# Optimization experiments

Hardware: AMD Instinct MI355X
Metric: run time of the kernel (lower is better)

Reference implementation:

```python
import jax, jax.numpy as jnp
import numpy as np

N1, N2, K = 262144, 65536, 16   # dense points, coarse points, knn neighbors
CIN, COUT = 64, 64              # in_planes, out_planes
EPS = 1e-5


def bn(x, g, b, m, v):
    # eval-mode BatchNorm1d with learned affine and running stats
    return (x - m) * jax.lax.rsqrt(v + EPS) * g + b


def setup_inputs() -> dict:
    key = jax.random.key(0)
    ks = jax.random.split(key, 32)
    u = lambda k, *s: jax.random.normal(k, s, jnp.float32)
    lin = lambda k, o, i: jax.random.normal(k, (o, i), jnp.float32) / np.float32(np.sqrt(i))
    inp = dict(
        p1=u(ks[0], N1, 3), p2=u(ks[1], N2, 3),
        x1=u(ks[2], N1, COUT), x2=u(ks[3], N2, CIN),
        knn_idx=jax.random.randint(ks[4], (N2, K), 0, N1),
        # linear1: Linear(COUT,COUT) + BN + ReLU
        w1=lin(ks[5], COUT, COUT), b1=0.01 * u(ks[6], COUT),
        g1=jnp.ones(COUT), be1=jnp.zeros(COUT),
        m1=0.1 * u(ks[7], COUT), v1=jax.random.uniform(ks[8], (COUT,), minval=0.5, maxval=1.5),
        # linear2: Linear(CIN,COUT) + BN + ReLU
        w2=lin(ks[9], COUT, CIN), b2=0.01 * u(ks[10], COUT),
        g2=jnp.ones(COUT), be2=jnp.zeros(COUT),
        m2=0.1 * u(ks[11], COUT), v2=jax.random.uniform(ks[12], (COUT,), minval=0.5, maxval=1.5),
        # channel_shrinker: Linear(CIN+3,CIN) + BN + ReLU + Linear(CIN,1)
        ws1=lin(ks[13], CIN, CIN + 3), bs1=0.01 * u(ks[14], CIN),
        gs=jnp.ones(CIN), bes=jnp.zeros(CIN),
        ms=0.1 * u(ks[15], CIN), vs=jax.random.uniform(ks[16], (CIN,), minval=0.5, maxval=1.5),
        ws2=lin(ks[17], 1, CIN), bs2=0.01 * u(ks[18], 1),
    )
    return inp


def reference(p1, p2, x1, x2, knn_idx,
              w1, b1, g1, be1, m1, v1,
              w2, b2, g2, be2, m2, v2,
              ws1, bs1, gs, bes, ms, vs, ws2, bs2):
    idx = knn_idx.reshape(-1)                                   # [M] = [N2*K], indices into p1
    # relative position of each knn neighbor to its coarse query point
    p_r = p1[idx].reshape(N2, K, 3) - p2[:, None, :]            # [N2,K,3]
    x2k = jnp.concatenate(
        [p_r, jnp.broadcast_to(x2[:, None, :], (N2, K, CIN))], axis=-1
    ).reshape(N2 * K, CIN + 3)                                  # [M, CIN+3]
    # channel_shrinker MLP -> scalar logit per (coarse, neighbor) pair
    h = jax.nn.relu(bn(x2k @ ws1.T + bs1, gs, bes, ms, vs))     # [M, CIN]
    logit = (h @ ws2.T + bs2)[:, 0]                             # [M]
    # scatter_softmax over variable in-degree groups keyed by dense point idx
    gmax = jax.lax.stop_gradient(jax.ops.segment_max(logit, idx, num_segments=N1))
    e = jnp.exp(logit - gmax[idx])
    denom = jax.ops.segment_sum(e, idx, num_segments=N1)
    prob = e / denom[idx]                                       # [M]
    # linear2(x2), broadcast over K neighbors, weight, scatter-sum to dense points
    up_feat = jax.nn.relu(bn(x2 @ w2.T + b2, g2, be2, m2, v2))  # [N2, COUT]
    weighted = (up_feat[:, None, :] * prob.reshape(N2, K, 1)).reshape(N2 * K, COUT)
    up = jax.ops.segment_sum(weighted, idx, num_segments=N1)    # [N1, COUT]
    # skip branch: linear1(x1)
    y1 = jax.nn.relu(bn(x1 @ w1.T + b1, g1, be1, m1, v1))       # [N1, COUT]
    return y1 + up
```

## Files before the change

### kernel.cpp

```cpp
#include <hip/hip_runtime.h>

#define CN1 262144
#define CN2 65536
#define CK  16
#define CM  (CN2*CK)

typedef unsigned short u16;
typedef unsigned int   u32;
typedef float f32x4 __attribute__((ext_vector_type(4)));

__device__ __forceinline__ float b2f(u16 h) {
    union { u32 u; float f; } v; v.u = ((u32)h) << 16; return v.f;
}
__device__ __forceinline__ u16 f2b(float f) {
    union { float f; u32 u; } v; v.f = f;
    u32 lsb = (v.u >> 16) & 1u;
    return (u16)((v.u + 0x7FFFu + lsb) >> 16);
}

#define W_POS   0
#define W_FT    256
#define W_AS    12544
#define W_BS    12608
#define W_WS2   12672
#define W_A2    12736
#define W_B2    12800
#define W_A1    12864
#define W_B1    12928
#define W_BS2   12992
#define W_MODE  13000
#define W_W1T   13056
#define W_W2T   17152
#define W_JP    21248

__device__ __forceinline__ float ldv(const void* p, size_t i, int bf) {
    return bf ? b2f(((const u16*)p)[i]) : ((const float*)p)[i];
}

#define DECL_ACC8 \
    f32x4 A0={0,0,0,0},A1={0,0,0,0},A2={0,0,0,0},A3={0,0,0,0}, \
          A4={0,0,0,0},A5={0,0,0,0},A6={0,0,0,0},A7={0,0,0,0};

#define FMA4(A, Wv) \
    (A).x = fmaf(xv_, (Wv).x, (A).x); (A).y = fmaf(xv_, (Wv).y, (A).y); \
    (A).z = fmaf(xv_, (Wv).z, (A).z); (A).w = fmaf(xv_, (Wv).w, (A).w);

#define WSTEP8(wtco, ivar, xval) { \
    float xv_ = (xval); \
    const f32x4* wr_ = (const f32x4*)((wtco) + ((size_t)(ivar) << 6)); \
    FMA4(A0, wr_[0])  FMA4(A1, wr_[1])  FMA4(A2, wr_[2])  FMA4(A3, wr_[3]) \
    FMA4(A4, wr_[4])  FMA4(A5, wr_[5])  FMA4(A6, wr_[6])  FMA4(A7, wr_[7]) }

#define GEMV32T(bf, xrow_f, xrow_u4, wtco) \
    if (bf) { \
        const uint4* xu_ = (xrow_u4); \
        _Pragma("unroll 2") \
        for (int ii_ = 0; ii_ < 8; ++ii_) { \
            uint4 xc_ = xu_[ii_]; \
            WSTEP8(wtco, ii_*8+0, b2f((u16)(xc_.x & 0xffffu))) \
            WSTEP8(wtco, ii_*8+1, b2f((u16)(xc_.x >> 16))) \
            WSTEP8(wtco, ii_*8+2, b2f((u16)(xc_.y & 0xffffu))) \
            WSTEP8(wtco, ii_*8+3, b2f((u16)(xc_.y >> 16))) \
            WSTEP8(wtco, ii_*8+4, b2f((u16)(xc_.z & 0xffffu))) \
            WSTEP8(wtco, ii_*8+5, b2f((u16)(xc_.z >> 16))) \
            WSTEP8(wtco, ii_*8+6, b2f((u16)(xc_.w & 0xffffu))) \
            WSTEP8(wtco, ii_*8+7, b2f((u16)(xc_.w >> 16))) \
        } \
    } else { \
        const float4* xf_ = (xrow_f); \
        _Pragma("unroll 2") \
        for (int ii_ = 0; ii_ < 8; ++ii_) { \
            float4 xa_ = xf_[2*ii_], xb_ = xf_[2*ii_+1]; \
            WSTEP8(wtco, ii_*8+0, xa_.x) WSTEP8(wtco, ii_*8+1, xa_.y) \
            WSTEP8(wtco, ii_*8+2, xa_.z) WSTEP8(wtco, ii_*8+3, xa_.w) \
            WSTEP8(wtco, ii_*8+4, xb_.x) WSTEP8(wtco, ii_*8+5, xb_.y) \
            WSTEP8(wtco, ii_*8+6, xb_.z) WSTEP8(wtco, ii_*8+7, xb_.w) \
        } \
    }

#define BNR1(A, av, bv) \
    (A).x = fmaxf(fmaf((A).x,(av).x,(bv).x),0.f); \
    (A).y = fmaxf(fmaf((A).y,(av).y,(bv).y),0.f); \
    (A).z = fmaxf(fmaf((A).z,(av).z,(bv).z),0.f); \
    (A).w = fmaxf(fmaf((A).w,(av).w,(bv).w),0.f);
#define BNR8(aBase, bBase) { \
    const f32x4* av_ = (const f32x4*)(aBase); \
    const f32x4* bv_ = (const f32x4*)(bBase); \
    BNR1(A0,av_[0],bv_[0]) BNR1(A1,av_[1],bv_[1]) \
    BNR1(A2,av_[2],bv_[2]) BNR1(A3,av_[3],bv_[3]) \
    BNR1(A4,av_[4],bv_[4]) BNR1(A5,av_[5],bv_[5]) \
    BNR1(A6,av_[6],bv_[6]) BNR1(A7,av_[7],bv_[7]) }

#define UFQ(q, AL, AH) { uint4 u_ = ufr_[q]; \
    (AL).x = fmaf(pe_, b2f((u16)(u_.x & 0xffffu)), (AL).x); \
    (AL).y = fmaf(pe_, b2f((u16)(u_.x >> 16)),     (AL).y); \
    (AL).z = fmaf(pe_, b2f((u16)(u_.y & 0xffffu)), (AL).z); \
    (AL).w = fmaf(pe_, b2f((u16)(u_.y >> 16)),     (AL).w); \
    (AH).x = fmaf(pe_, b2f((u16)(u_.z & 0xffffu)), (AH).x); \
    (AH).y = fmaf(pe_, b2f((u16)(u_.z >> 16)),     (AH).y); \
    (AH).z = fmaf(pe_, b2f((u16)(u_.w & 0xffffu)), (AH).z); \
    (AH).w = fmaf(pe_, b2f((u16)(u_.w >> 16)),     (AH).w); }

#define STQ(q, AL, AH, dst) { uint4 o_; \
    o_.x = (u32)f2b((AL).x) | ((u32)f2b((AL).y) << 16); \
    o_.y = (u32)f2b((AL).z) | ((u32)f2b((AL).w) << 16); \
    o_.z = (u32)f2b((AH).x) | ((u32)f2b((AH).y) << 16); \
    o_.w = (u32)f2b((AH).z) | ((u32)f2b((AH).w) << 16); \
    ((uint4*)(dst))[q] = o_; }
#define STORE_BF8(dst) \
    STQ(0,A0,A1,dst) STQ(1,A2,A3,dst) STQ(2,A4,A5,dst) STQ(3,A6,A7,dst)
#define STORE_F328(dst) { f32x4* ov_ = (f32x4*)(dst); \
    ov_[0]=A0; ov_[1]=A1; ov_[2]=A2; ov_[3]=A3; \
    ov_[4]=A4; ov_[5]=A5; ov_[6]=A6; ov_[7]=A7; }

__global__ __launch_bounds__(256) void k_prep(
    const void* __restrict__ w1,  const void* __restrict__ b1,  const void* __restrict__ g1,
    const void* __restrict__ be1, const void* __restrict__ m1,  const void* __restrict__ v1,
    const void* __restrict__ w2,  const void* __restrict__ b2,  const void* __restrict__ g2,
    const void* __restrict__ be2, const void* __restrict__ m2,  const void* __restrict__ v2,
    const void* __restrict__ ws1, const void* __restrict__ bs1, const void* __restrict__ gs,
    const void* __restrict__ bes, const void* __restrict__ ms,  const void* __restrict__ vs,
    const void* __restrict__ ws2, const void* __restrict__ bs2, float* __restrict__ wb,
    u32* __restrict__ offsets, u32* __restrict__ cursor)
{
    int b = blockIdx.x;
    int tid = threadIdx.x;
    if (b > 0) {
        offsets[(b - 1) * 256 + tid] = 0u;
        if (b == 1 && tid == 0) *cursor = 0u;
        return;
    }

    u32 w0 = ((const u32*)g1)[0];
    int bf = (w0 != 0x3F800000u) ? 1 : 0;

    for (int t = tid; t < 64*64; t += 256) {
        int i = t >> 6, c = t & 63;
        wb[W_FT  + t] = ldv(ws1, (size_t)c*67 + 3 + i, bf);
        wb[W_W1T + t] = ldv(w1,  (size_t)c*64 + i, bf);
        wb[W_W2T + t] = ldv(w2,  (size_t)c*64 + i, bf);
    }
    for (int t = tid; t < 64*3; t += 256) {
        int j = t / 3, k = t % 3;
        wb[W_POS + t] = ldv(ws1, (size_t)j*67 + k, bf);
    }
    if (tid < 64) {
        float as = ldv(gs, tid, bf) * rsqrtf(ldv(vs, tid, bf) + 1e-5f);
        float bs = (ldv(bs1, tid, bf) - ldv(ms, tid, bf)) * as + ldv(bes, tid, bf);
        float wc = ldv(ws2, tid, bf);
        wb[W_AS + tid] = as;
        wb[W_BS + tid] = bs;
        wb[W_WS2 + tid] = wc;
        float a2 = ldv(g2, tid, bf) * rsqrtf(ldv(v2, tid, bf) + 1e-5f);
        wb[W_A2 + tid] = a2;
        wb[W_B2 + tid] = (ldv(b2, tid, bf) - ldv(m2, tid, bf)) * a2 + ldv(be2, tid, bf);
        float a1 = ldv(g1, tid, bf) * rsqrtf(ldv(v1, tid, bf) + 1e-5f);
        wb[W_A1 + tid] = a1;
        wb[W_B1 + tid] = (ldv(b1, tid, bf) - ldv(m1, tid, bf)) * a1 + ldv(be1, tid, bf);
        wb[W_JP + tid*8 + 0] = ldv(ws1, (size_t)tid*67 + 0, bf);
        wb[W_JP + tid*8 + 1] = ldv(ws1, (size_t)tid*67 + 1, bf);
        wb[W_JP + tid*8 + 2] = ldv(ws1, (size_t)tid*67 + 2, bf);
        wb[W_JP + tid*8 + 3] = as;
        wb[W_JP + tid*8 + 4] = bs;
        wb[W_JP + tid*8 + 5] = wc;
        wb[W_JP + tid*8 + 6] = 0.f;
        wb[W_JP + tid*8 + 7] = 0.f;
    }
    if (tid == 0) {
        wb[W_BS2] = ldv(bs2, 0, bf);
        ((u32*)wb)[W_MODE] = (u32)bf;
    }
}

__global__ __launch_bounds__(256, 8) void k_coarse2(
    const void* __restrict__ x2, const int* __restrict__ knn,
    const float* __restrict__ wb,
    float* __restrict__ dots, u16* __restrict__ upfeat,
    u32* __restrict__ offsets)
{
    int bf   = (int)((const u32*)wb)[W_MODE];
    int tid  = threadIdx.x;
    int role = blockIdx.x & 1;
    int lane = tid & 63;
    int co   = __builtin_amdgcn_readfirstlane(((tid >> 6) & 1) << 5);
    int n2   = (blockIdx.x >> 1) * 128 + (tid >> 7) * 64 + lane;
    const float4* xf = (const float4*)((const float*)x2 + (size_t)n2 * 64);
    const uint4*  xu = (const uint4*)((const u16*)x2 + (size_t)n2 * 64);

    if (role == 0) {
        if (co == 0) {
            const int4* kv = (const int4*)(knn + (size_t)n2 * 16);
            #pragma unroll
            for (int q = 0; q < 4; q++) {
                int4 t = kv[q];
                atomicAdd(&offsets[t.x & (CN1-1)], 1u);
                atomicAdd(&offsets[t.y & (CN1-1)], 1u);
                atomicAdd(&offsets[t.z & (CN1-1)], 1u);
                atomicAdd(&offsets[t.w & (CN1-1)], 1u);
            }
        }
        DECL_ACC8
        GEMV32T(bf, xf, xu, wb + W_FT + co)
        STORE_F328(dots + (size_t)n2 * 64 + co)
    } else {
        DECL_ACC8
        GEMV32T(bf, xf, xu, wb + W_W2T + co)
        BNR8(wb + W_A2 + co, wb + W_B2 + co)
        STORE_BF8(upfeat + (size_t)n2 * 64 + co)
    }
}

__global__ __launch_bounds__(256) void k_scan(
    u32* __restrict__ offsets, u32* __restrict__ cursor)
{
    __shared__ u32 s[256];
    __shared__ u32 base;
    int t = threadIdx.x;
    int i = blockIdx.x * 256 + t;
    u32 v = offsets[i];
    s[t] = v; __syncthreads();
    for (int off = 1; off < 256; off <<= 1) {
        u32 add = (t >= off) ? s[t-off] : 0u;
        __syncthreads();
        s[t] += add;
        __syncthreads();
    }
    u32 inc = s[t];
    if (t == 255) base = atomicAdd(cursor, inc);
    __syncthreads();
    offsets[i] = (base + inc - v) << 6;
}

#define LSTEP(j, dv) { f32x4 pa_ = jp[2*(j)], pb_ = jp[2*(j)+1]; \
    float pre_ = fmaf(prz, pa_.z, fmaf(pry, pa_.y, fmaf(prx, pa_.x, (dv)))); \
    float h_ = fmaxf(fmaf(pre_, pa_.w, pb_.x), 0.f); \
    lg = fmaf(h_, pb_.y, lg); }

__global__ __launch_bounds__(256) void k_logit_scatter(
    const void* __restrict__ p1, const void* __restrict__ p2,
    const int* __restrict__ knn, const float* __restrict__ wb,
    const float* __restrict__ dots,
    float* __restrict__ logits, u32* __restrict__ offsets,
    u32* __restrict__ csr)
{
    int bf = (int)((const u32*)wb)[W_MODE];
    int m  = blockIdx.x * 256 + threadIdx.x;
    int n2 = m >> 4;

    int idx = knn[m] & (CN1-1);

    u32 v = atomicAdd(&offsets[idx], 1u);
    u32 pos = (v >> 6) + (v & 63u);
    csr[pos & (CM-1)] = (u32)m;

    float prx = ldv(p1, (size_t)idx*3+0, bf) - ldv(p2, (size_t)n2*3+0, bf);
    float pry = ldv(p1, (size_t)idx*3+1, bf) - ldv(p2, (size_t)n2*3+1, bf);
    float prz = ldv(p1, (size_t)idx*3+2, bf) - ldv(p2, (size_t)n2*3+2, bf);

    const f32x4*  jp  = (const f32x4*)(wb + W_JP);
    const float4* dr4 = (const float4*)(dots + (size_t)n2 * 64);
    float lg = 0.f;
    #pragma unroll 4
    for (int jq = 0; jq < 16; ++jq) {
        float4 d4 = dr4[jq];
        LSTEP(jq*4+0, d4.x) LSTEP(jq*4+1, d4.y)
        LSTEP(jq*4+2, d4.z) LSTEP(jq*4+3, d4.w)
    }
    logits[m] = lg + wb[W_BS2];
}

__global__ __launch_bounds__(256, 8) void k_dense(
    const void* __restrict__ x1, const float* __restrict__ wb,
    const float* __restrict__ logits, const u16* __restrict__ upfeat,
    const u32* __restrict__ offsets, const u32* __restrict__ csr,
    void* __restrict__ out)
{
    int bf   = (int)((const u32*)wb)[W_MODE];
    int tid  = threadIdx.x;
    int lane = tid & 63;
    int co   = __builtin_amdgcn_readfirstlane(((tid >> 6) & 1) << 5);
    int n1   = blockIdx.x * 128 + (tid >> 7) * 64 + lane;

    u32 pk = offsets[n1];
    int d = (int)(pk & 63u);
    int start = (int)(pk >> 6);

    float mxv = -3.0e38f, s = 0.f;
    for (int e = 0; e < d; ++e) {
        u32 m = csr[(u32)(start + e) & (CM-1)] & (CM-1);
        float l = logits[m];
        float mnew = fmaxf(mxv, l);
        s = fmaf(s, __expf(mxv - mnew), __expf(l - mnew));
        mxv = mnew;
    }
    float inv = (d > 0) ? (1.f / s) : 0.f;

    DECL_ACC8
    GEMV32T(bf, (const float4*)((const float*)x1 + (size_t)n1 * 64),
                (const uint4*)((const u16*)x1 + (size_t)n1 * 64),
                wb + W_W1T + co)
    BNR8(wb + W_A1 + co, wb + W_B1 + co)

    for (int e = 0; e < d; ++e) {
        u32 m = csr[(u32)(start + e) & (CM-1)] & (CM-1);
        float pe_ = __expf(logits[m] - mxv) * inv;
        const uint4* ufr_ = (const uint4*)(upfeat + (size_t)(m >> 4) * 64 + co);
        UFQ(0,A0,A1) UFQ(1,A2,A3) UFQ(2,A4,A5) UFQ(3,A6,A7)
    }

    if (bf) { u16* orow = (u16*)out + (size_t)n1 * 64 + co; STORE_BF8(orow) }
    else    { STORE_F328((float*)out + (size_t)n1 * 64 + co) }
}

extern "C" void kernel_launch(void* const* d_in, const int* in_sizes, int n_in,
                              void* d_out, int out_size, void* d_ws, size_t ws_size,
                              hipStream_t stream)
{
    (void)in_sizes; (void)n_in; (void)out_size; (void)ws_size;
    const void* p1   = d_in[0];
    const void* p2   = d_in[1];
    const void* x1   = d_in[2];
    const void* x2   = d_in[3];
    const int*  knn  = (const int*)d_in[4];
    const void* w1   = d_in[5];
    const void* b1   = d_in[6];
    const void* g1   = d_in[7];
    const void* be1  = d_in[8];
    const void* m1   = d_in[9];
    const void* v1   = d_in[10];
    const void* w2   = d_in[11];
    const void* b2   = d_in[12];
    const void* g2   = d_in[13];
    const void* be2  = d_in[14];
    const void* m2   = d_in[15];
    const void* v2   = d_in[16];
    const void* ws1  = d_in[17];
    const void* bs1  = d_in[18];
    const void* gs   = d_in[19];
    const void* bes  = d_in[20];
    const void* ms   = d_in[21];
    const void* vs   = d_in[22];
    const void* ws2w = d_in[23];
    const void* bs2  = d_in[24];

    char* ws = (char*)d_ws;
    float* wb      = (float*)(ws);
    float* logits  = (float*)(ws + ((size_t)1  << 20));
    u32*   csr     = (u32*)  (ws + ((size_t)5  << 20));
    u16*   upfeat  = (u16*)  (ws + ((size_t)9  << 20));
    u32*   offsets = (u32*)  (ws + ((size_t)17 << 20));
    u32*   cursor  = (u32*)  (ws + ((size_t)18 << 20));
    float* dots    = (float*)d_out;

    k_prep          <<<1 + CN1/256, 256, 0, stream>>>(w1,b1,g1,be1,m1,v1,
                                                      w2,b2,g2,be2,m2,v2,
                                                      ws1,bs1,gs,bes,ms,vs,
                                                      ws2w, bs2, wb, offsets, cursor);
    k_coarse2       <<<2*(CN2/128), 256, 0, stream>>>(x2, knn, wb, dots, upfeat, offsets);
    k_scan          <<<CN1/256,     256, 0, stream>>>(offsets, cursor);
    k_logit_scatter <<<CM/256,      256, 0, stream>>>(p1, p2, knn, wb, dots,
                                                      logits, offsets, csr);
    k_dense         <<<CN1/128,     256, 0, stream>>>(x1, wb, logits, upfeat,
                                                      offsets, csr, d_out);
}
```

Baseline: 230.3 us.

## Store logits in CSR order and restructure dense kernel with prefetched gathers

The logit-scatter kernel now writes each logit at its CSR slot, so the dense kernel's softmax pass reads logits contiguously instead of through an indirect csr lookup. The dense kernel maps one thread per dense point and loops over both 32-channel halves in-thread, with a one-step software prefetch of the next neighbor's upfeat row and logit. Launch bounds drop to 4 waves per SIMD to allow more registers. The aim is to cut random gathers and hide gather latency, at the cost of lower occupancy and the x1 row being read twice per thread.

```diff
diff --git a/kernel.cpp b/kernel.cpp
--- a/kernel.cpp
+++ b/kernel.cpp
@@ -37,13 +37,13 @@
     return bf ? b2f(((const u16*)p)[i]) : ((const float*)p)[i];
 }
 
+#define FMA4(A, Wv) \
+    (A).x = fmaf(xv_, (Wv).x, (A).x); (A).y = fmaf(xv_, (Wv).y, (A).y); \
+    (A).z = fmaf(xv_, (Wv).z, (A).z); (A).w = fmaf(xv_, (Wv).w, (A).w);
+
 #define DECL_ACC8 \
     f32x4 A0={0,0,0,0},A1={0,0,0,0},A2={0,0,0,0},A3={0,0,0,0}, \
           A4={0,0,0,0},A5={0,0,0,0},A6={0,0,0,0},A7={0,0,0,0};
-
-#define FMA4(A, Wv) \
-    (A).x = fmaf(xv_, (Wv).x, (A).x); (A).y = fmaf(xv_, (Wv).y, (A).y); \
-    (A).z = fmaf(xv_, (Wv).z, (A).z); (A).w = fmaf(xv_, (Wv).w, (A).w);
 
 #define WSTEP8(wtco, ivar, xval) { \
     float xv_ = (xval); \
@@ -91,15 +91,15 @@
     BNR1(A4,av_[4],bv_[4]) BNR1(A5,av_[5],bv_[5]) \
     BNR1(A6,av_[6],bv_[6]) BNR1(A7,av_[7],bv_[7]) }
 
-#define UFQ(q, AL, AH) { uint4 u_ = ufr_[q]; \
-    (AL).x = fmaf(pe_, b2f((u16)(u_.x & 0xffffu)), (AL).x); \
-    (AL).y = fmaf(pe_, b2f((u16)(u_.x >> 16)),     (AL).y); \
-    (AL).z = fmaf(pe_, b2f((u16)(u_.y & 0xffffu)), (AL).z); \
-    (AL).w = fmaf(pe_, b2f((u16)(u_.y >> 16)),     (AL).w); \
-    (AH).x = fmaf(pe_, b2f((u16)(u_.z & 0xffffu)), (AH).x); \
-    (AH).y = fmaf(pe_, b2f((u16)(u_.z >> 16)),     (AH).y); \
-    (AH).z = fmaf(pe_, b2f((u16)(u_.w & 0xffffu)), (AH).z); \
-    (AH).w = fmaf(pe_, b2f((u16)(u_.w >> 16)),     (AH).w); }
+#define UFR(u_, AL, AH) { \
+    (AL).x = fmaf(pe_, b2f((u16)((u_).x & 0xffffu)), (AL).x); \
+    (AL).y = fmaf(pe_, b2f((u16)((u_).x >> 16)),     (AL).y); \
+    (AL).z = fmaf(pe_, b2f((u16)((u_).y & 0xffffu)), (AL).z); \
+    (AL).w = fmaf(pe_, b2f((u16)((u_).y >> 16)),     (AL).w); \
+    (AH).x = fmaf(pe_, b2f((u16)((u_).z & 0xffffu)), (AH).x); \
+    (AH).y = fmaf(pe_, b2f((u16)((u_).z >> 16)),     (AH).y); \
+    (AH).z = fmaf(pe_, b2f((u16)((u_).w & 0xffffu)), (AH).z); \
+    (AH).w = fmaf(pe_, b2f((u16)((u_).w >> 16)),     (AH).w); }
 
 #define STQ(q, AL, AH, dst) { uint4 o_; \
     o_.x = (u32)f2b((AL).x) | ((u32)f2b((AL).y) << 16); \
@@ -107,7 +107,7 @@
     o_.z = (u32)f2b((AH).x) | ((u32)f2b((AH).y) << 16); \
     o_.w = (u32)f2b((AH).z) | ((u32)f2b((AH).w) << 16); \
     ((uint4*)(dst))[q] = o_; }
-#define STORE_BF8(dst) \
+#define STORE_BF8V(dst) \
     STQ(0,A0,A1,dst) STQ(1,A2,A3,dst) STQ(2,A4,A5,dst) STQ(3,A6,A7,dst)
 #define STORE_F328(dst) { f32x4* ov_ = (f32x4*)(dst); \
     ov_[0]=A0; ov_[1]=A1; ov_[2]=A2; ov_[3]=A3; \
@@ -206,7 +206,7 @@
         DECL_ACC8
         GEMV32T(bf, xf, xu, wb + W_W2T + co)
         BNR8(wb + W_A2 + co, wb + W_B2 + co)
-        STORE_BF8(upfeat + (size_t)n2 * 64 + co)
+        STORE_BF8V(upfeat + (size_t)n2 * 64 + co)
     }
 }
 
@@ -240,7 +240,7 @@
     const void* __restrict__ p1, const void* __restrict__ p2,
     const int* __restrict__ knn, const float* __restrict__ wb,
     const float* __restrict__ dots,
-    float* __restrict__ logits, u32* __restrict__ offsets,
+    float* __restrict__ logitc, u32* __restrict__ offsets,
     u32* __restrict__ csr)
 {
     int bf = (int)((const u32*)wb)[W_MODE];
@@ -250,8 +250,8 @@
     int idx = knn[m] & (CN1-1);
 
     u32 v = atomicAdd(&offsets[idx], 1u);
-    u32 pos = (v >> 6) + (v & 63u);
-    csr[pos & (CM-1)] = (u32)m;
+    u32 pos = ((v >> 6) + (v & 63u)) & (CM-1);
+    csr[pos] = (u32)m;
 
     float prx = ldv(p1, (size_t)idx*3+0, bf) - ldv(p2, (size_t)n2*3+0, bf);
     float pry = ldv(p1, (size_t)idx*3+1, bf) - ldv(p2, (size_t)n2*3+1, bf);
@@ -266,20 +266,17 @@
         LSTEP(jq*4+0, d4.x) LSTEP(jq*4+1, d4.y)
         LSTEP(jq*4+2, d4.z) LSTEP(jq*4+3, d4.w)
     }
-    logits[m] = lg + wb[W_BS2];
-}
-
-__global__ __launch_bounds__(256, 8) void k_dense(
+    logitc[pos] = lg + wb[W_BS2];
+}
+
+__global__ __launch_bounds__(256, 4) void k_dense(
     const void* __restrict__ x1, const float* __restrict__ wb,
-    const float* __restrict__ logits, const u16* __restrict__ upfeat,
+    const float* __restrict__ logitc, const u16* __restrict__ upfeat,
     const u32* __restrict__ offsets, const u32* __restrict__ csr,
     void* __restrict__ out)
 {
-    int bf   = (int)((const u32*)wb)[W_MODE];
-    int tid  = threadIdx.x;
-    int lane = tid & 63;
-    int co   = __builtin_amdgcn_readfirstlane(((tid >> 6) & 1) << 5);
-    int n1   = blockIdx.x * 128 + (tid >> 7) * 64 + lane;
+    int bf = (int)((const u32*)wb)[W_MODE];
+    int n1 = blockIdx.x * 256 + threadIdx.x;
 
     u32 pk = offsets[n1];
     int d = (int)(pk & 63u);
@@ -287,29 +284,46 @@
 
     float mxv = -3.0e38f, s = 0.f;
     for (int e = 0; e < d; ++e) {
-        u32 m = csr[(u32)(start + e) & (CM-1)] & (CM-1);
-        float l = logits[m];
+        float l = logitc[(u32)(start + e) & (CM-1)];
         float mnew = fmaxf(mxv, l);
         s = fmaf(s, __expf(mxv - mnew), __expf(l - mnew));
         mxv = mnew;
     }
     float inv = (d > 0) ? (1.f / s) : 0.f;
 
-    DECL_ACC8
-    GEMV32T(bf, (const float4*)((const float*)x1 + (size_t)n1 * 64),
-                (const uint4*)((const u16*)x1 + (size_t)n1 * 64),
-                wb + W_W1T + co)
-    BNR8(wb + W_A1 + co, wb + W_B1 + co)
-
-    for (int e = 0; e < d; ++e) {
-        u32 m = csr[(u32)(start + e) & (CM-1)] & (CM-1);
-        float pe_ = __expf(logits[m] - mxv) * inv;
-        const uint4* ufr_ = (const uint4*)(upfeat + (size_t)(m >> 4) * 64 + co);
-        UFQ(0,A0,A1) UFQ(1,A2,A3) UFQ(2,A4,A5) UFQ(3,A6,A7)
-    }
-
-    if (bf) { u16* orow = (u16*)out + (size_t)n1 * 64 + co; STORE_BF8(orow) }
-    else    { STORE_F328((float*)out + (size_t)n1 * 64 + co) }
+    const float4* xf = (const float4*)((const float*)x1 + (size_t)n1 * 64);
+    const uint4*  xu = (const uint4*)((const u16*)x1 + (size_t)n1 * 64);
+
+    #pragma unroll 1
+    for (int pass = 0; pass < 2; ++pass) {
+        int co = __builtin_amdgcn_readfirstlane(pass << 5);
+
+        DECL_ACC8
+        GEMV32T(bf, xf, xu, wb + W_W1T + co)
+        BNR8(wb + W_A1 + co, wb + W_B1 + co)
+
+        u32 q0 = (u32)start & (CM-1);
+        u32 mc = csr[q0] & (CM-1);
+        float lc = logitc[q0];
+        const uint4* upc = (const uint4*)(upfeat + (size_t)(mc >> 4) * 64 + co);
+        uint4 r0 = upc[0], r1 = upc[1], r2 = upc[2], r3 = upc[3];
+
+        for (int e = 0; e < d; ++e) {
+            u32 qn = (u32)(start + e + 1) & (CM-1);
+            u32 mn = csr[qn] & (CM-1);
+            float ln = logitc[qn];
+            const uint4* upn = (const uint4*)(upfeat + (size_t)(mn >> 4) * 64 + co);
+            uint4 s0 = upn[0], s1 = upn[1], s2 = upn[2], s3 = upn[3];
+
+            float pe_ = __expf(lc - mxv) * inv;
+            UFR(r0, A0, A1) UFR(r1, A2, A3) UFR(r2, A4, A5) UFR(r3, A6, A7)
+
+            r0 = s0; r1 = s1; r2 = s2; r3 = s3; lc = ln;
+        }
+
+        if (bf) { u16* orow = (u16*)out + (size_t)n1 * 64 + co; STORE_BF8V(orow) }
+        else    { STORE_F328((float*)out + (size_t)n1 * 64 + co) }
+    }
 }
 
 extern "C" void kernel_launch(void* const* d_in, const int* in_sizes, int n_in,
@@ -345,7 +359,7 @@
 
     char* ws = (char*)d_ws;
     float* wb      = (float*)(ws);
-    float* logits  = (float*)(ws + ((size_t)1  << 20));
+    float* logitc  = (float*)(ws + ((size_t)1  << 20));
     u32*   csr     = (u32*)  (ws + ((size_t)5  << 20));
     u16*   upfeat  = (u16*)  (ws + ((size_t)9  << 20));
     u32*   offsets = (u32*)  (ws + ((size_t)17 << 20));
@@ -359,7 +373,7 @@
     k_coarse2       <<<2*(CN2/128), 256, 0, stream>>>(x2, knn, wb, dots, upfeat, offsets);
     k_scan          <<<CN1/256,     256, 0, stream>>>(offsets, cursor);
     k_logit_scatter <<<CM/256,      256, 0, stream>>>(p1, p2, knn, wb, dots,
-                                                      logits, offsets, csr);
-    k_dense         <<<CN1/128,     256, 0, stream>>>(x1, wb, logits, upfeat,
+                                                      logitc, offsets, csr);
+    k_dense         <<<CN1/256,     256, 0, stream>>>(x1, wb, logitc, upfeat,
                                                       offsets, csr, d_out);
 }
```

After: 229.7 us. About the same (-0.3%).
